# Optimization experiments

Measured on AMD Instinct MI355X. Metric: run time of the kernel, lower is better.

## Reference

```python
import jax, jax.numpy as jnp
import numpy as np

B, S, D = 4, 8192, 1024
H = 16
HD = D // H          # 64
AD = 64              # approx_dim
EPS = 1e-6


def setup_inputs() -> dict:
    key = jax.random.key(0)
    ks = jax.random.split(key, 5)
    x = jax.random.normal(ks[0], (B, S, D), dtype=jnp.float32)
    # qkv_proj: Linear(D, 3*D)
    W_qkv = jax.random.normal(ks[1], (3 * D, D), dtype=jnp.float32) * (1.0 / np.sqrt(D))
    b_qkv = jnp.zeros((3 * D,), dtype=jnp.float32)
    # proj: Linear(HD, AD) with xavier_uniform init, zero bias
    limit = np.sqrt(6.0 / (HD + AD))
    W_p = jax.random.uniform(ks[2], (AD, HD), dtype=jnp.float32, minval=-limit, maxval=limit)
    b_p = jnp.zeros((AD,), dtype=jnp.float32)
    return {"x": x, "W_qkv": W_qkv, "b_qkv": b_qkv, "W_p": W_p, "b_p": b_p}


def reference(x, W_qkv, b_qkv, W_p, b_p):
    # qkv projection and split
    qkv = x @ W_qkv.T + b_qkv                      # [B,S,3D]
    Q, K, V = jnp.split(qkv, 3, axis=-1)
    # [B,S,D] -> [B,H,S,HD]
    def to_heads(t):
        return t.reshape(B, S, H, HD).transpose(0, 2, 1, 3)
    Q, K, V = to_heads(Q), to_heads(K), to_heads(V)
    # shared projection to approx dim, feature map phi(u) = sqrt(1 + u^2)
    pQ = jnp.einsum('bhsd,ad->bhsa', Q, W_p) + b_p
    pK = jnp.einsum('bhsd,ad->bhsa', K, W_p) + b_p
    phi_Q = jnp.sqrt(1.0 + pQ * pQ)                # [B,H,S,AD]
    phi_K = jnp.sqrt(1.0 + pK * pK)
    # linear attention: O(S) chained contractions
    KTV = jnp.einsum('bhsa,bhsv->bhav', phi_K, V)  # [B,H,AD,HD]
    numerator = jnp.einsum('bhsa,bhav->bhsv', phi_Q, KTV)  # [B,H,S,HD]
    k_sum = phi_K.sum(axis=2)                      # [B,H,AD]
    denominator = jnp.einsum('bhsa,bha->bhs', phi_Q, k_sum)  # [B,H,S]
    head_out = numerator / (denominator[..., None] + EPS)
    # [B,H,S,HD] -> [B,S,D]
    return head_out.transpose(0, 2, 1, 3).reshape(B, S, D)
```

## Files before the change

### kernel.cpp

```cpp
#include <hip/hip_runtime.h>
#include <hip/hip_bf16.h>
#include <cstdint>

static constexpr int Bc  = 4;
static constexpr int Sc  = 8192;
static constexpr int Dc  = 1024;
static constexpr int Hc  = 16;
static constexpr int BHc = Bc * Hc;
static constexpr int Mc  = Bc * Sc;
static constexpr int N3c = 3 * Dc;
static constexpr float EPSc = 1e-6f;

using bf16x8 = __attribute__((ext_vector_type(8))) __bf16;
using f32x4  = __attribute__((ext_vector_type(4))) float;

__device__ __forceinline__ ushort f2bf(float f) {
  union { float f; uint32_t u; } v; v.f = f;
  uint32_t u = v.u;
  return (ushort)((u + 0x7fffu + ((u >> 16) & 1u)) >> 16);
}
__device__ __forceinline__ float bf2f(ushort h) {
  union { uint32_t u; float f; } v; v.u = ((uint32_t)h) << 16;
  return v.f;
}

typedef const __attribute__((address_space(1))) unsigned int* gas_u32p;
typedef __attribute__((address_space(3))) unsigned int* las_u32p;
__device__ __forceinline__ void gld_lds16(const void* g, void* l) {
  __builtin_amdgcn_global_load_lds((gas_u32p)g, (las_u32p)l, 16, 0, 0);
}

__global__ __launch_bounds__(256) void prep_k(const float* __restrict__ x,
                                              ushort* __restrict__ xb,
                                              const float* __restrict__ Wq,
                                              const float* __restrict__ Wp,
                                              const float* __restrict__ bq,
                                              const float* __restrict__ bp,
                                              ushort* __restrict__ W3b,
                                              float* __restrict__ bias3) {
  const int t = threadIdx.x;
  if (blockIdx.x < 2048) {
    const int n4 = Mc * Dc / 4;
    for (int i = blockIdx.x * 256 + t; i < n4; i += 2048 * 256) {
      float4 v = reinterpret_cast<const float4*>(x)[i];
      ushort4 o; o.x = f2bf(v.x); o.y = f2bf(v.y); o.z = f2bf(v.z); o.w = f2bf(v.w);
      reinterpret_cast<ushort4*>(xb)[i] = o;
    }
    return;
  }
  const int bx = blockIdx.x - 2048;
  const int p = bx >> 4, h = bx & 15;
  if (p == 2) {
    const int base = 2048 + h * 64;
    for (int li = t; li < 64 * 256; li += 256) {
      int r = li >> 8, c4 = (li & 255) * 4;
      float4 v = *reinterpret_cast<const float4*>(&Wq[(size_t)(base + r) * 1024 + c4]);
      ushort4 o; o.x = f2bf(v.x); o.y = f2bf(v.y); o.z = f2bf(v.z); o.w = f2bf(v.w);
      *reinterpret_cast<ushort4*>(&W3b[(size_t)(base + r) * 1024 + c4]) = o;
    }
    if (t < 64) bias3[base + t] = bq[base + t];
    return;
  }
  __shared__ ushort Ws[64 * 64];
  __shared__ ushort Tq[256 * 64];
  const int rbase = p * 1024 + h * 64;
  for (int li = t; li < 64 * 16; li += 256) {
    int a = li >> 4, h4 = (li & 15) * 4;
    float4 v = *reinterpret_cast<const float4*>(&Wp[a * 64 + h4]);
    ushort4 o; o.x = f2bf(v.x); o.y = f2bf(v.y); o.z = f2bf(v.z); o.w = f2bf(v.w);
    *reinterpret_cast<ushort4*>(&Ws[a * 64 + h4]) = o;
  }
  if (t < 64) {
    float s = bp[t];
    for (int hd = 0; hd < 64; ++hd) s += Wp[t * 64 + hd] * bq[rbase + hd];
    bias3[rbase + t] = s;
  }
  const int w = t >> 6, lane = t & 63, lr = lane & 15, kg = lane >> 4;
  for (int dt = 0; dt < 4; ++dt) {
    __syncthreads();
    for (int li = t; li < 64 * 64; li += 256) {
      int hd = li >> 6, d4 = (li & 63) * 4;
      float4 v = *reinterpret_cast<const float4*>(&Wq[(size_t)(rbase + hd) * 1024 + dt * 256 + d4]);
      Tq[(d4 + 0) * 64 + hd] = f2bf(v.x);
      Tq[(d4 + 1) * 64 + hd] = f2bf(v.y);
      Tq[(d4 + 2) * 64 + hd] = f2bf(v.z);
      Tq[(d4 + 3) * 64 + hd] = f2bf(v.w);
    }
    __syncthreads();
    f32x4 acc[4][4];
#pragma unroll
    for (int i = 0; i < 4; i++)
#pragma unroll
      for (int j = 0; j < 4; j++) acc[i][j] = (f32x4){0.f, 0.f, 0.f, 0.f};
#pragma unroll
    for (int kk = 0; kk < 2; ++kk) {
      bf16x8 af[4], bfr[4];
#pragma unroll
      for (int i = 0; i < 4; i++)
        af[i] = *reinterpret_cast<const bf16x8*>(&Ws[(i * 16 + lr) * 64 + kk * 32 + kg * 8]);
#pragma unroll
      for (int j = 0; j < 4; j++)
        bfr[j] = *reinterpret_cast<const bf16x8*>(&Tq[(w * 64 + j * 16 + lr) * 64 + kk * 32 + kg * 8]);
#pragma unroll
      for (int i = 0; i < 4; i++)
#pragma unroll
        for (int j = 0; j < 4; j++)
          acc[i][j] = __builtin_amdgcn_mfma_f32_16x16x32_bf16(af[i], bfr[j], acc[i][j], 0, 0, 0);
    }
#pragma unroll
    for (int i = 0; i < 4; i++)
#pragma unroll
      for (int j = 0; j < 4; j++)
#pragma unroll
        for (int r = 0; r < 4; r++)
          W3b[(size_t)(rbase + i * 16 + kg * 4 + r) * 1024 + dt * 256 + w * 64 + j * 16 + lr] =
              f2bf(acc[i][j][r]);
  }
}

__global__ __launch_bounds__(512, 2) void gemm_kv_k(const ushort* __restrict__ xb,
                                                    const ushort* __restrict__ W3b,
                                                    const float* __restrict__ bias3,
                                                    ushort* __restrict__ KTb,
                                                    ushort* __restrict__ VTb) {
  __shared__ __align__(16) ushort As[4 * 8192];
  __shared__ __align__(16) ushort Bs[4 * 8192];
  const int t = threadIdx.x, wave = t >> 6, lane = t & 63;
  const int lr = lane & 15, kg = lane >> 4;
  const int wr = wave >> 2, wc = wave & 3;

  const int flat = blockIdx.x;
  const int swz  = (flat & 7) * 128 + (flat >> 3);
  const int n0 = 1024 + (swz % 8) * 256;
  const int m0 = (swz / 8) * 256;

  const int srow = t >> 2;
  const int sg   = (t & 3) ^ ((t >> 3) & 3);
  const int swb  = wave * 512;

  auto STAGE = [&](int tile, int buf) {
    const int kt = tile * 32;
#pragma unroll
    for (int is = 0; is < 2; ++is) {
      gld_lds16(xb  + (size_t)(m0 + is * 128 + srow) * 1024 + kt + sg * 8,
                As + buf * 8192 + is * 4096 + swb);
      gld_lds16(W3b + (size_t)(n0 + is * 128 + srow) * 1024 + kt + sg * 8,
                Bs + buf * 8192 + is * 4096 + swb);
    }
  };

  f32x4 acc[8][4];
#pragma unroll
  for (int f = 0; f < 8; f++)
#pragma unroll
    for (int j = 0; j < 4; j++) acc[f][j] = (f32x4){0.f, 0.f, 0.f, 0.f};

  const int cp = (kg ^ ((lr >> 1) & 3)) * 8;
  const ushort* Ard = As + (wr * 128 + lr) * 32 + cp;
  const ushort* Brd = Bs + (wc * 64 + lr) * 32 + cp;

  auto COMPUTE = [&](int buf) {
    bf16x8 af[8], bfr[4];
    const ushort* Ab = Ard + buf * 8192;
    const ushort* Bb = Brd + buf * 8192;
#pragma unroll
    for (int f = 0; f < 8; f++) af[f] = *reinterpret_cast<const bf16x8*>(Ab + f * 512);
#pragma unroll
    for (int j = 0; j < 4; j++) bfr[j] = *reinterpret_cast<const bf16x8*>(Bb + j * 512);
    __builtin_amdgcn_s_setprio(1);
#pragma unroll
    for (int f = 0; f < 8; f++)
#pragma unroll
      for (int j = 0; j < 4; j++)
        acc[f][j] = __builtin_amdgcn_mfma_f32_16x16x32_bf16(af[f], bfr[j], acc[f][j], 0, 0, 0);
    __builtin_amdgcn_s_setprio(0);
  };

  STAGE(0, 0);
  STAGE(1, 1);
  STAGE(2, 2);
  asm volatile("s_waitcnt vmcnt(8)" ::: "memory");
  __builtin_amdgcn_s_barrier();

#pragma unroll 1
  for (int i = 0; i < 7; ++i) {
    const int tb = i * 4;
#pragma unroll
    for (int j = 0; j < 4; ++j) {
      STAGE(tb + j + 3, (j + 3) & 3);
      COMPUTE(j);
      asm volatile("s_waitcnt vmcnt(8)" ::: "memory");
      __builtin_amdgcn_s_barrier();
    }
  }
  STAGE(31, 3);
  COMPUTE(0);
  asm volatile("s_waitcnt vmcnt(8)" ::: "memory");
  __builtin_amdgcn_s_barrier();
  COMPUTE(1);
  asm volatile("s_waitcnt vmcnt(4)" ::: "memory");
  __builtin_amdgcn_s_barrier();
  COMPUTE(2);
  asm volatile("s_waitcnt vmcnt(0)" ::: "memory");
  __builtin_amdgcn_s_barrier();
  COMPUTE(3);

  const int n0w  = n0 + wc * 64;
  const int part = n0w >> 10;
  const int h    = (n0w & 1023) >> 6;
  const int bq   = m0 >> 13;
  const int s_base = (m0 & 8191) + wr * 128;
  float bias[4];
#pragma unroll
  for (int j = 0; j < 4; j++) bias[j] = bias3[n0w + j * 16 + lr];

  ushort* dst = ((part == 1) ? KTb : VTb) + ((size_t)(bq * Hc + h)) * 64 * Sc;
#pragma unroll
  for (int f = 0; f < 8; f++) {
    const int s = s_base + f * 16 + kg * 4;
#pragma unroll
    for (int j = 0; j < 4; j++) {
      ushort4 o;
      if (part == 1) {
#pragma unroll
        for (int r = 0; r < 4; r++) {
          float p = acc[f][j][r] + bias[j];
          (&o.x)[r] = f2bf(sqrtf(1.f + p * p));
        }
      } else {
#pragma unroll
        for (int r = 0; r < 4; r++) (&o.x)[r] = f2bf(acc[f][j][r] + bias[j]);
      }
      *reinterpret_cast<ushort4*>(&dst[(size_t)(j * 16 + lr) * Sc + s]) = o;
    }
  }
}

__global__ __launch_bounds__(256, 2) void ktv_part_k(const ushort* __restrict__ KT,
                                                     const ushort* __restrict__ VT,
                                                     float* __restrict__ KTVp,
                                                     float* __restrict__ ksump) {
  __shared__ __align__(16) ushort Ks[2 * 8192];
  __shared__ __align__(16) ushort Vs[2 * 8192];
  const int t = threadIdx.x, chunk = blockIdx.x, bh = blockIdx.y;
  const int wave = t >> 6, lane = t & 63, lr = lane & 15, kg = lane >> 4;
  const size_t hb = (size_t)bh * 64 * Sc;
  const int s0 = chunk * 1024;

  f32x4 acc[4];
  f32x4 acc_ks;
#pragma unroll
  for (int j = 0; j < 4; j++) acc[j] = (f32x4){0.f, 0.f, 0.f, 0.f};
  acc_ks = (f32x4){0.f, 0.f, 0.f, 0.f};

  bf16x8 ones;
#pragma unroll
  for (int e = 0; e < 8; e++) ones[e] = (__bf16)1.0f;

  const int srl = t >> 4;
  const int scc = (t & 15) ^ ((t >> 4) & 7);
  const int wb  = (t >> 6) * 512;

  auto STG = [&](int st, int buf) {
    const int sb = s0 + st * 128;
#pragma unroll
    for (int is = 0; is < 4; ++is) {
      const int row = is * 16 + srl;
      gld_lds16(KT + hb + (size_t)row * Sc + sb + scc * 8, Ks + buf * 8192 + is * 2048 + wb);
      gld_lds16(VT + hb + (size_t)row * Sc + sb + scc * 8, Vs + buf * 8192 + is * 2048 + wb);
    }
  };

  auto COMPUTE = [&](int buf) {
    const ushort* Kb = Ks + buf * 8192;
    const ushort* Vb = Vs + buf * 8192;
#pragma unroll
    for (int ks4 = 0; ks4 < 4; ++ks4) {
      const int pos = ((ks4 * 4 + kg) ^ (lr & 7)) * 8;
      bf16x8 af = *reinterpret_cast<const bf16x8*>(Kb + (wave * 16 + lr) * 128 + pos);
      acc_ks = __builtin_amdgcn_mfma_f32_16x16x32_bf16(af, ones, acc_ks, 0, 0, 0);
#pragma unroll
      for (int j = 0; j < 4; ++j) {
        bf16x8 bv = *reinterpret_cast<const bf16x8*>(Vb + (j * 16 + lr) * 128 + pos);
        acc[j] = __builtin_amdgcn_mfma_f32_16x16x32_bf16(af, bv, acc[j], 0, 0, 0);
      }
    }
  };

  STG(0, 0);
  __syncthreads();
#pragma unroll 1
  for (int st = 0; st < 8; ++st) {
    if (st < 7) STG(st + 1, (st + 1) & 1);
    COMPUTE(st & 1);
    __syncthreads();
  }

  float* outp = KTVp + ((size_t)bh * 8 + chunk) * 4096;
#pragma unroll
  for (int j = 0; j < 4; ++j)
#pragma unroll
    for (int r = 0; r < 4; ++r)
      outp[(wave * 16 + kg * 4 + r) * 64 + j * 16 + lr] = acc[j][r];
  if (lr == 0) {
#pragma unroll
    for (int r = 0; r < 4; ++r)
      ksump[((size_t)bh * 8 + chunk) * 64 + wave * 16 + kg * 4 + r] = acc_ks[r];
  }
}

__global__ __launch_bounds__(256) void ktv_red_k(const float* __restrict__ KTVp,
                                                 const float* __restrict__ ksump,
                                                 ushort* __restrict__ KTVTb,
                                                 float* __restrict__ ksum) {
  const int bh = blockIdx.x, t = threadIdx.x;
  for (int li = t; li < 4096; li += 256) {
    const int v = li >> 6, a = li & 63;
    float s = 0.f;
    for (int c = 0; c < 8; c++) s += KTVp[((size_t)bh * 8 + c) * 4096 + a * 64 + v];
    KTVTb[(size_t)bh * 4096 + li] = f2bf(s);
  }
  if (t < 64) {
    float s = 0.f;
    for (int c = 0; c < 8; c++) s += ksump[((size_t)bh * 8 + c) * 64 + t];
    ksum[bh * 64 + t] = s;
  }
}

__global__ __launch_bounds__(512, 2) void gemm_q_k(const ushort* __restrict__ xb,
                                                   const ushort* __restrict__ W3b,
                                                   const float* __restrict__ bias3,
                                                   const ushort* __restrict__ KTVTb,
                                                   const float* __restrict__ ksum,
                                                   float* __restrict__ out) {
  __shared__ __align__(16) ushort As[4 * 8192];
  __shared__ __align__(16) ushort Bs[4 * 8192];
  const int t = threadIdx.x, wave = t >> 6, lane = t & 63;
  const int lr = lane & 15, kg = lane >> 4;
  const int wr = wave >> 2, wc = wave & 3;

  const int flat = blockIdx.x;
  const int swz  = (flat & 7) * 64 + (flat >> 3);
  const int n0 = (swz % 4) * 256;
  const int m0 = (swz / 4) * 256;

  const int srow = t >> 2;
  const int sg   = (t & 3) ^ ((t >> 3) & 3);
  const int swb  = wave * 512;

  auto STAGE = [&](int tile, int buf) {
    const int kt = tile * 32;
#pragma unroll
    for (int is = 0; is < 2; ++is) {
      gld_lds16(xb  + (size_t)(m0 + is * 128 + srow) * 1024 + kt + sg * 8,
                As + buf * 8192 + is * 4096 + swb);
      gld_lds16(W3b + (size_t)(n0 + is * 128 + srow) * 1024 + kt + sg * 8,
                Bs + buf * 8192 + is * 4096 + swb);
    }
  };

  f32x4 acc[8][4];
#pragma unroll
  for (int f = 0; f < 8; f++)
#pragma unroll
    for (int j = 0; j < 4; j++) acc[f][j] = (f32x4){0.f, 0.f, 0.f, 0.f};

  const int cp = (kg ^ ((lr >> 1) & 3)) * 8;
  const ushort* Ard = As + (wr * 128 + lr) * 32 + cp;
  const ushort* Brd = Bs + (wc * 64 + lr) * 32 + cp;

  auto COMPUTE = [&](int buf) {
    bf16x8 af[8], bfr[4];
    const ushort* Ab = Ard + buf * 8192;
    const ushort* Bb = Brd + buf * 8192;
#pragma unroll
    for (int f = 0; f < 8; f++) af[f] = *reinterpret_cast<const bf16x8*>(Ab + f * 512);
#pragma unroll
    for (int j = 0; j < 4; j++) bfr[j] = *reinterpret_cast<const bf16x8*>(Bb + j * 512);
    __builtin_amdgcn_s_setprio(1);
#pragma unroll
    for (int f = 0; f < 8; f++)
#pragma unroll
      for (int j = 0; j < 4; j++)
        acc[f][j] = __builtin_amdgcn_mfma_f32_16x16x32_bf16(af[f], bfr[j], acc[f][j], 0, 0, 0);
    __builtin_amdgcn_s_setprio(0);
  };

  STAGE(0, 0);
  STAGE(1, 1);
  STAGE(2, 2);
  asm volatile("s_waitcnt vmcnt(8)" ::: "memory");
  __builtin_amdgcn_s_barrier();

#pragma unroll 1
  for (int i = 0; i < 7; ++i) {
    const int tb = i * 4;
#pragma unroll
    for (int j = 0; j < 4; ++j) {
      STAGE(tb + j + 3, (j + 3) & 3);
      COMPUTE(j);
      asm volatile("s_waitcnt vmcnt(8)" ::: "memory");
      __builtin_amdgcn_s_barrier();
    }
  }
  STAGE(31, 3);
  COMPUTE(0);
  asm volatile("s_waitcnt vmcnt(8)" ::: "memory");
  __builtin_amdgcn_s_barrier();
  COMPUTE(1);
  asm volatile("s_waitcnt vmcnt(4)" ::: "memory");
  __builtin_amdgcn_s_barrier();
  COMPUTE(2);
  asm volatile("s_waitcnt vmcnt(0)" ::: "memory");
  __builtin_amdgcn_s_barrier();
  COMPUTE(3);

  const int n0w = n0 + wc * 64;
  const int h   = n0w >> 6;
  const int bq  = m0 >> 13;
  const int bh  = bq * Hc + h;
  const int s_base = (m0 & 8191) + wr * 128;
  float bias[4];
#pragma unroll
  for (int j = 0; j < 4; j++) bias[j] = bias3[n0w + j * 16 + lr];

  __syncthreads();
  ushort* ep = (wave < 4) ? (As + wave * 8192) : (Bs + (wave - 4) * 8192);

#pragma unroll
  for (int f = 0; f < 8; f++)
#pragma unroll
    for (int j = 0; j < 4; j++) {
      const int g = j * 2 + (lr >> 3);
      const int cl = lr & 7;
#pragma unroll
      for (int r = 0; r < 4; r++) {
        const int row = f * 16 + kg * 4 + r;
        float p = acc[f][j][r] + bias[j];
        ep[row * 64 + ((g ^ (row & 7)) << 3) + cl] = f2bf(sqrtf(1.f + p * p));
      }
    }

  bf16x8 bfr[4][2];
#pragma unroll
  for (int j = 0; j < 4; j++)
#pragma unroll
    for (int ks = 0; ks < 2; ks++)
      bfr[j][ks] = *reinterpret_cast<const bf16x8*>(
          &KTVTb[(size_t)bh * 4096 + (j * 16 + lr) * 64 + ks * 32 + kg * 8]);
  float ksc[2][8];
#pragma unroll
  for (int ks = 0; ks < 2; ks++) {
    float4 v0 = *reinterpret_cast<const float4*>(&ksum[bh * 64 + ks * 32 + kg * 8]);
    float4 v1 = *reinterpret_cast<const float4*>(&ksum[bh * 64 + ks * 32 + kg * 8 + 4]);
    ksc[ks][0] = v0.x; ksc[ks][1] = v0.y; ksc[ks][2] = v0.z; ksc[ks][3] = v0.w;
    ksc[ks][4] = v1.x; ksc[ks][5] = v1.y; ksc[ks][6] = v1.z; ksc[ks][7] = v1.w;
  }

#pragma unroll 1
  for (int f = 0; f < 8; f++) {
    bf16x8 af[2];
#pragma unroll
    for (int ks = 0; ks < 2; ks++)
      af[ks] = *reinterpret_cast<const bf16x8*>(
          &ep[(f * 16 + lr) * 64 + (((ks * 4 + kg) ^ (lr & 7)) << 3)]);
    float d = 0.f;
#pragma unroll
    for (int ks = 0; ks < 2; ks++)
#pragma unroll
      for (int e = 0; e < 8; e++) d += (float)af[ks][e] * ksc[ks][e];
    d += __shfl_xor(d, 16, 64);
    d += __shfl_xor(d, 32, 64);
    float den[4];
#pragma unroll
    for (int r = 0; r < 4; r++) den[r] = __shfl(d, kg * 4 + r, 64) + EPSc;
    f32x4 nacc[4];
#pragma unroll
    for (int j = 0; j < 4; j++) nacc[j] = (f32x4){0.f, 0.f, 0.f, 0.f};
#pragma unroll
    for (int ks = 0; ks < 2; ks++)
#pragma unroll
      for (int j = 0; j < 4; j++)
        nacc[j] = __builtin_amdgcn_mfma_f32_16x16x32_bf16(af[ks], bfr[j][ks], nacc[j], 0, 0, 0);
#pragma unroll
    for (int j = 0; j < 4; j++)
#pragma unroll
      for (int r = 0; r < 4; r++) {
        const int s = s_base + f * 16 + kg * 4 + r;
        out[((size_t)bq * Sc + s) * 1024 + h * 64 + j * 16 + lr] = nacc[j][r] / den[r];
      }
  }
}

extern "C" void kernel_launch(void* const* d_in, const int* in_sizes, int n_in,
                              void* d_out, int out_size, void* d_ws, size_t ws_size,
                              hipStream_t stream) {
  const float* x     = (const float*)d_in[0];
  const float* W_qkv = (const float*)d_in[1];
  const float* b_qkv = (const float*)d_in[2];
  const float* W_p   = (const float*)d_in[3];
  const float* b_p   = (const float*)d_in[4];
  float* out = (float*)d_out;

  size_t off = 0;
  auto carve = [&](size_t bytes) -> void* {
    void* p = (char*)d_ws + off;
    off += (bytes + 255) & ~(size_t)255;
    return p;
  };
  const size_t headElems = (size_t)BHc * Sc * 64;
  ushort* xb    = (ushort*)carve((size_t)Mc * Dc * 2);
  ushort* KTb   = (ushort*)carve(headElems * 2);
  ushort* VTb   = (ushort*)carve(headElems * 2);
  ushort* W3b   = (ushort*)carve((size_t)N3c * Dc * 2);
  float*  bias3 = (float*)carve((size_t)N3c * 4);
  float*  KTVp  = (float*)carve((size_t)BHc * 8 * 4096 * 4);
  float*  ksmp  = (float*)carve((size_t)BHc * 8 * 64 * 4);
  ushort* KTVTb = (ushort*)carve((size_t)BHc * 4096 * 2);
  float*  ksum  = (float*)carve((size_t)BHc * 64 * 4);
  (void)ws_size; (void)n_in; (void)in_sizes; (void)out_size;

  prep_k<<<2096, 256, 0, stream>>>(x, xb, W_qkv, W_p, b_qkv, b_p, W3b, bias3);
  gemm_kv_k<<<(Mc / 256) * (2048 / 256), 512, 0, stream>>>(xb, W3b, bias3, KTb, VTb);
  ktv_part_k<<<dim3(8, BHc), 256, 0, stream>>>(KTb, VTb, KTVp, ksmp);
  ktv_red_k<<<BHc, 256, 0, stream>>>(KTVp, ksmp, KTVTb, ksum);
  gemm_q_k<<<(Mc / 256) * (1024 / 256), 512, 0, stream>>>(xb, W3b, bias3, KTVTb, ksum, out);
}
```

Measured before the change: 383.8 us.

## Switch GEMM mainloops to double-buffered BK=64 tiles with 8-way swizzle

Both the K/V and Q projection GEMMs now stage 64-wide K tiles into two LDS buffers instead of 32-wide tiles into four. The LDS swizzle changes to an 8-chunk XOR pattern and each compute step issues two MFMA k-substeps per tile. This halves the number of barrier and wait rounds per K loop and gives longer MFMA bursts per barrier. The cost is a shallower prefetch distance (one tile ahead instead of three), which may expose more global load latency.

```diff
diff --git a/kernel.cpp b/kernel.cpp
--- a/kernel.cpp
+++ b/kernel.cpp
@@ -118,13 +118,14 @@
   }
 }
 
+
 __global__ __launch_bounds__(512, 2) void gemm_kv_k(const ushort* __restrict__ xb,
                                                     const ushort* __restrict__ W3b,
                                                     const float* __restrict__ bias3,
                                                     ushort* __restrict__ KTb,
                                                     ushort* __restrict__ VTb) {
-  __shared__ __align__(16) ushort As[4 * 8192];
-  __shared__ __align__(16) ushort Bs[4 * 8192];
+  __shared__ __align__(16) ushort As[2 * 16384];
+  __shared__ __align__(16) ushort Bs[2 * 16384];
   const int t = threadIdx.x, wave = t >> 6, lane = t & 63;
   const int lr = lane & 15, kg = lane >> 4;
   const int wr = wave >> 2, wc = wave & 3;
@@ -134,18 +135,18 @@
   const int n0 = 1024 + (swz % 8) * 256;
   const int m0 = (swz / 8) * 256;
 
-  const int srow = t >> 2;
-  const int sg   = (t & 3) ^ ((t >> 3) & 3);
-  const int swb  = wave * 512;
+  const int srow8 = lane >> 3;
+  const int sg    = (lane & 7) ^ ((lane >> 3) & 7);
 
   auto STAGE = [&](int tile, int buf) {
-    const int kt = tile * 32;
-#pragma unroll
-    for (int is = 0; is < 2; ++is) {
-      gld_lds16(xb  + (size_t)(m0 + is * 128 + srow) * 1024 + kt + sg * 8,
-                As + buf * 8192 + is * 4096 + swb);
-      gld_lds16(W3b + (size_t)(n0 + is * 128 + srow) * 1024 + kt + sg * 8,
-                Bs + buf * 8192 + is * 4096 + swb);
+    const int kt = tile * 64;
+#pragma unroll
+    for (int i = 0; i < 4; ++i) {
+      const int r0 = (wave * 4 + i) * 8;
+      gld_lds16(xb  + (size_t)(m0 + r0 + srow8) * 1024 + kt + sg * 8,
+                As + buf * 16384 + (wave * 4 + i) * 512);
+      gld_lds16(W3b + (size_t)(n0 + r0 + srow8) * 1024 + kt + sg * 8,
+                Bs + buf * 16384 + (wave * 4 + i) * 512);
     }
   };
 
@@ -155,55 +156,54 @@
 #pragma unroll
     for (int j = 0; j < 4; j++) acc[f][j] = (f32x4){0.f, 0.f, 0.f, 0.f};
 
-  const int cp = (kg ^ ((lr >> 1) & 3)) * 8;
-  const ushort* Ard = As + (wr * 128 + lr) * 32 + cp;
-  const ushort* Brd = Bs + (wc * 64 + lr) * 32 + cp;
-
   auto COMPUTE = [&](int buf) {
-    bf16x8 af[8], bfr[4];
-    const ushort* Ab = Ard + buf * 8192;
-    const ushort* Bb = Brd + buf * 8192;
-#pragma unroll
-    for (int f = 0; f < 8; f++) af[f] = *reinterpret_cast<const bf16x8*>(Ab + f * 512);
-#pragma unroll
-    for (int j = 0; j < 4; j++) bfr[j] = *reinterpret_cast<const bf16x8*>(Bb + j * 512);
-    __builtin_amdgcn_s_setprio(1);
-#pragma unroll
-    for (int f = 0; f < 8; f++)
+    const ushort* Ab = As + buf * 16384;
+    const ushort* Bb = Bs + buf * 16384;
+#pragma unroll
+    for (int kk = 0; kk < 2; ++kk) {
+      const int cp = ((kk * 4 + kg) ^ (lr & 7)) * 8;
+      bf16x8 af[8], bfr[4];
+#pragma unroll
+      for (int f = 0; f < 8; f++)
+        af[f] = *reinterpret_cast<const bf16x8*>(Ab + (wr * 128 + f * 16 + lr) * 64 + cp);
 #pragma unroll
       for (int j = 0; j < 4; j++)
-        acc[f][j] = __builtin_amdgcn_mfma_f32_16x16x32_bf16(af[f], bfr[j], acc[f][j], 0, 0, 0);
-    __builtin_amdgcn_s_setprio(0);
+        bfr[j] = *reinterpret_cast<const bf16x8*>(Bb + (wc * 64 + j * 16 + lr) * 64 + cp);
+      __builtin_amdgcn_s_setprio(1);
+#pragma unroll
+      for (int f = 0; f < 8; f++)
+#pragma unroll
+        for (int j = 0; j < 4; j++)
+          acc[f][j] = __builtin_amdgcn_mfma_f32_16x16x32_bf16(af[f], bfr[j], acc[f][j], 0, 0, 0);
+      __builtin_amdgcn_s_setprio(0);
+    }
   };
 
   STAGE(0, 0);
-  STAGE(1, 1);
-  STAGE(2, 2);
+#pragma unroll 1
+  for (int tt = 0; tt < 7; ++tt) {
+    STAGE(tt * 2 + 1, 1);
+    asm volatile("s_waitcnt vmcnt(8)" ::: "memory");
+    __builtin_amdgcn_s_barrier();
+    COMPUTE(0);
+    asm volatile("" ::: "memory");
+    __builtin_amdgcn_s_barrier();
+    STAGE(tt * 2 + 2, 0);
+    asm volatile("s_waitcnt vmcnt(8)" ::: "memory");
+    __builtin_amdgcn_s_barrier();
+    COMPUTE(1);
+    asm volatile("" ::: "memory");
+    __builtin_amdgcn_s_barrier();
+  }
+  STAGE(15, 1);
   asm volatile("s_waitcnt vmcnt(8)" ::: "memory");
   __builtin_amdgcn_s_barrier();
-
-#pragma unroll 1
-  for (int i = 0; i < 7; ++i) {
-    const int tb = i * 4;
-#pragma unroll
-    for (int j = 0; j < 4; ++j) {
-      STAGE(tb + j + 3, (j + 3) & 3);
-      COMPUTE(j);
-      asm volatile("s_waitcnt vmcnt(8)" ::: "memory");
-      __builtin_amdgcn_s_barrier();
-    }
-  }
-  STAGE(31, 3);
   COMPUTE(0);
-  asm volatile("s_waitcnt vmcnt(8)" ::: "memory");
+  asm volatile("" ::: "memory");
+  __builtin_amdgcn_s_barrier();
+  asm volatile("s_waitcnt vmcnt(0)" ::: "memory");
   __builtin_amdgcn_s_barrier();
   COMPUTE(1);
-  asm volatile("s_waitcnt vmcnt(4)" ::: "memory");
-  __builtin_amdgcn_s_barrier();
-  COMPUTE(2);
-  asm volatile("s_waitcnt vmcnt(0)" ::: "memory");
-  __builtin_amdgcn_s_barrier();
-  COMPUTE(3);
 
   const int n0w  = n0 + wc * 64;
   const int part = n0w >> 10;
@@ -333,8 +333,8 @@
                                                    const ushort* __restrict__ KTVTb,
                                                    const float* __restrict__ ksum,
                                                    float* __restrict__ out) {
-  __shared__ __align__(16) ushort As[4 * 8192];
-  __shared__ __align__(16) ushort Bs[4 * 8192];
+  __shared__ __align__(16) ushort As[2 * 16384];
+  __shared__ __align__(16) ushort Bs[2 * 16384];
   const int t = threadIdx.x, wave = t >> 6, lane = t & 63;
   const int lr = lane & 15, kg = lane >> 4;
   const int wr = wave >> 2, wc = wave & 3;
@@ -344,18 +344,18 @@
   const int n0 = (swz % 4) * 256;
   const int m0 = (swz / 4) * 256;
 
-  const int srow = t >> 2;
-  const int sg   = (t & 3) ^ ((t >> 3) & 3);
-  const int swb  = wave * 512;
+  const int srow8 = lane >> 3;
+  const int sg    = (lane & 7) ^ ((lane >> 3) & 7);
 
   auto STAGE = [&](int tile, int buf) {
-    const int kt = tile * 32;
-#pragma unroll
-    for (int is = 0; is < 2; ++is) {
-      gld_lds16(xb  + (size_t)(m0 + is * 128 + srow) * 1024 + kt + sg * 8,
-                As + buf * 8192 + is * 4096 + swb);
-      gld_lds16(W3b + (size_t)(n0 + is * 128 + srow) * 1024 + kt + sg * 8,
-                Bs + buf * 8192 + is * 4096 + swb);
+    const int kt = tile * 64;
+#pragma unroll
+    for (int i = 0; i < 4; ++i) {
+      const int r0 = (wave * 4 + i) * 8;
+      gld_lds16(xb  + (size_t)(m0 + r0 + srow8) * 1024 + kt + sg * 8,
+                As + buf * 16384 + (wave * 4 + i) * 512);
+      gld_lds16(W3b + (size_t)(n0 + r0 + srow8) * 1024 + kt + sg * 8,
+                Bs + buf * 16384 + (wave * 4 + i) * 512);
     }
   };
 
@@ -365,55 +365,54 @@
 #pragma unroll
     for (int j = 0; j < 4; j++) acc[f][j] = (f32x4){0.f, 0.f, 0.f, 0.f};
 
-  const int cp = (kg ^ ((lr >> 1) & 3)) * 8;
-  const ushort* Ard = As + (wr * 128 + lr) * 32 + cp;
-  const ushort* Brd = Bs + (wc * 64 + lr) * 32 + cp;
-
   auto COMPUTE = [&](int buf) {
-    bf16x8 af[8], bfr[4];
-    const ushort* Ab = Ard + buf * 8192;
-    const ushort* Bb = Brd + buf * 8192;
-#pragma unroll
-    for (int f = 0; f < 8; f++) af[f] = *reinterpret_cast<const bf16x8*>(Ab + f * 512);
-#pragma unroll
-    for (int j = 0; j < 4; j++) bfr[j] = *reinterpret_cast<const bf16x8*>(Bb + j * 512);
-    __builtin_amdgcn_s_setprio(1);
-#pragma unroll
-    for (int f = 0; f < 8; f++)
+    const ushort* Ab = As + buf * 16384;
+    const ushort* Bb = Bs + buf * 16384;
+#pragma unroll
+    for (int kk = 0; kk < 2; ++kk) {
+      const int cp = ((kk * 4 + kg) ^ (lr & 7)) * 8;
+      bf16x8 af[8], bfr[4];
+#pragma unroll
+      for (int f = 0; f < 8; f++)
+        af[f] = *reinterpret_cast<const bf16x8*>(Ab + (wr * 128 + f * 16 + lr) * 64 + cp);
 #pragma unroll
       for (int j = 0; j < 4; j++)
-        acc[f][j] = __builtin_amdgcn_mfma_f32_16x16x32_bf16(af[f], bfr[j], acc[f][j], 0, 0, 0);
-    __builtin_amdgcn_s_setprio(0);
+        bfr[j] = *reinterpret_cast<const bf16x8*>(Bb + (wc * 64 + j * 16 + lr) * 64 + cp);
+      __builtin_amdgcn_s_setprio(1);
+#pragma unroll
+      for (int f = 0; f < 8; f++)
+#pragma unroll
+        for (int j = 0; j < 4; j++)
+          acc[f][j] = __builtin_amdgcn_mfma_f32_16x16x32_bf16(af[f], bfr[j], acc[f][j], 0, 0, 0);
+      __builtin_amdgcn_s_setprio(0);
+    }
   };
 
   STAGE(0, 0);
-  STAGE(1, 1);
-  STAGE(2, 2);
+#pragma unroll 1
+  for (int tt = 0; tt < 7; ++tt) {
+    STAGE(tt * 2 + 1, 1);
+    asm volatile("s_waitcnt vmcnt(8)" ::: "memory");
+    __builtin_amdgcn_s_barrier();
+    COMPUTE(0);
+    asm volatile("" ::: "memory");
+    __builtin_amdgcn_s_barrier();
+    STAGE(tt * 2 + 2, 0);
+    asm volatile("s_waitcnt vmcnt(8)" ::: "memory");
+    __builtin_amdgcn_s_barrier();
+    COMPUTE(1);
+    asm volatile("" ::: "memory");
+    __builtin_amdgcn_s_barrier();
+  }
+  STAGE(15, 1);
   asm volatile("s_waitcnt vmcnt(8)" ::: "memory");
   __builtin_amdgcn_s_barrier();
-
-#pragma unroll 1
-  for (int i = 0; i < 7; ++i) {
-    const int tb = i * 4;
-#pragma unroll
-    for (int j = 0; j < 4; ++j) {
-      STAGE(tb + j + 3, (j + 3) & 3);
-      COMPUTE(j);
-      asm volatile("s_waitcnt vmcnt(8)" ::: "memory");
-      __builtin_amdgcn_s_barrier();
-    }
-  }
-  STAGE(31, 3);
   COMPUTE(0);
-  asm volatile("s_waitcnt vmcnt(8)" ::: "memory");
+  asm volatile("" ::: "memory");
+  __builtin_amdgcn_s_barrier();
+  asm volatile("s_waitcnt vmcnt(0)" ::: "memory");
   __builtin_amdgcn_s_barrier();
   COMPUTE(1);
-  asm volatile("s_waitcnt vmcnt(4)" ::: "memory");
-  __builtin_amdgcn_s_barrier();
-  COMPUTE(2);
-  asm volatile("s_waitcnt vmcnt(0)" ::: "memory");
-  __builtin_amdgcn_s_barrier();
-  COMPUTE(3);
 
   const int n0w = n0 + wc * 64;
   const int h   = n0w >> 6;
```

Result: no change. 389.7 us (+1.5%).

## Restructure KV GEMM mainloop into double-buffered 64-wide K tiles with interleaved staging

Applied to the files above, without the earlier changes.

The KV projection GEMM now uses two buffers of 64-wide K tiles, each split into two 32-wide halves, in place of a four-deep ring of 32-wide tiles. Each tile is computed in four quarter steps of 16 MFMAs. Staging loads for the next tile are placed between those steps, separated by compiler-fenced barriers, so LDS reads, global-to-LDS copies and MFMA work interleave more finely. The cost is a shallower prefetch depth and many more barriers per tile, which can leave waves stalled on synchronisation.

```diff
diff --git a/kernel.cpp b/kernel.cpp
--- a/kernel.cpp
+++ b/kernel.cpp
@@ -29,6 +29,8 @@
 __device__ __forceinline__ void gld_lds16(const void* g, void* l) {
   __builtin_amdgcn_global_load_lds((gas_u32p)g, (las_u32p)l, 16, 0, 0);
 }
+
+#define BARF do { asm volatile("" ::: "memory"); __builtin_amdgcn_s_barrier(); asm volatile("" ::: "memory"); } while (0)
 
 __global__ __launch_bounds__(256) void prep_k(const float* __restrict__ x,
                                               ushort* __restrict__ xb,
@@ -138,6 +140,235 @@
   const int sg   = (t & 3) ^ ((t >> 3) & 3);
   const int swb  = wave * 512;
 
+  auto stgA = [&](int tile, int kh) {
+    const int col = tile * 64 + kh * 32 + sg * 8;
+    ushort* dst = As + ((tile & 1) * 2 + kh) * 8192 + swb;
+    gld_lds16(xb + (size_t)(m0 + srow) * 1024 + col, dst);
+    gld_lds16(xb + (size_t)(m0 + 128 + srow) * 1024 + col, dst + 4096);
+  };
+  auto stgB = [&](int tile, int kh) {
+    const int col = tile * 64 + kh * 32 + sg * 8;
+    ushort* dst = Bs + ((tile & 1) * 2 + kh) * 8192 + swb;
+    gld_lds16(W3b + (size_t)(n0 + srow) * 1024 + col, dst);
+    gld_lds16(W3b + (size_t)(n0 + 128 + srow) * 1024 + col, dst + 4096);
+  };
+
+  f32x4 acc[8][4];
+#pragma unroll
+  for (int f = 0; f < 8; f++)
+#pragma unroll
+    for (int j = 0; j < 4; j++) acc[f][j] = (f32x4){0.f, 0.f, 0.f, 0.f};
+
+  const int cp = (kg ^ ((lr >> 1) & 3)) * 8;
+  bf16x8 bfr[4];
+
+  auto readA4 = [&](bf16x8* af, int buf, int fh, int kk) {
+#pragma unroll
+    for (int f = 0; f < 4; f++)
+      af[f] = *reinterpret_cast<const bf16x8*>(
+          As + (buf * 2 + kk) * 8192 + (wr * 128 + fh * 64 + f * 16 + lr) * 32 + cp);
+  };
+  auto readB4 = [&](int buf, int kk) {
+#pragma unroll
+    for (int j = 0; j < 4; j++)
+      bfr[j] = *reinterpret_cast<const bf16x8*>(
+          Bs + (buf * 2 + kk) * 8192 + (wc * 64 + j * 16 + lr) * 32 + cp);
+  };
+  auto mfma16 = [&](const bf16x8* af, int fh) {
+    __builtin_amdgcn_s_setprio(1);
+#pragma unroll
+    for (int f = 0; f < 4; f++)
+#pragma unroll
+      for (int j = 0; j < 4; j++)
+        acc[fh * 4 + f][j] =
+            __builtin_amdgcn_mfma_f32_16x16x32_bf16(af[f], bfr[j], acc[fh * 4 + f][j], 0, 0, 0);
+    __builtin_amdgcn_s_setprio(0);
+  };
+
+  auto TILE = [&](int T, int buf, bool st) {
+    bf16x8 af[4];
+    readB4(buf, 0);
+    readA4(af, buf, 0, 0);
+    if (st) stgA(T + 1, 0);
+    BARF;
+    mfma16(af, 0);
+    BARF;
+    readA4(af, buf, 1, 0);
+    if (st) stgB(T + 1, 0);
+    BARF;
+    mfma16(af, 1);
+    if (st) asm volatile("s_waitcnt vmcnt(4)" ::: "memory");
+    else    asm volatile("s_waitcnt vmcnt(0)" ::: "memory");
+    BARF;
+    readB4(buf, 1);
+    readA4(af, buf, 0, 1);
+    if (st) stgA(T + 1, 1);
+    BARF;
+    mfma16(af, 0);
+    BARF;
+    readA4(af, buf, 1, 1);
+    if (st) stgB(T + 1, 1);
+    BARF;
+    mfma16(af, 1);
+    if (st) asm volatile("s_waitcnt vmcnt(4)" ::: "memory");
+    BARF;
+  };
+
+  stgA(0, 0); stgB(0, 0); stgA(0, 1); stgB(0, 1);
+  asm volatile("s_waitcnt vmcnt(4)" ::: "memory");
+  BARF;
+
+#pragma unroll 1
+  for (int tt = 0; tt < 7; ++tt) {
+    TILE(tt * 2, 0, true);
+    TILE(tt * 2 + 1, 1, true);
+  }
+  TILE(14, 0, true);
+  TILE(15, 1, false);
+
+  const int n0w  = n0 + wc * 64;
+  const int part = n0w >> 10;
+  const int h    = (n0w & 1023) >> 6;
+  const int bq   = m0 >> 13;
+  const int s_base = (m0 & 8191) + wr * 128;
+  float bias[4];
+#pragma unroll
+  for (int j = 0; j < 4; j++) bias[j] = bias3[n0w + j * 16 + lr];
+
+  ushort* dst = ((part == 1) ? KTb : VTb) + ((size_t)(bq * Hc + h)) * 64 * Sc;
+#pragma unroll
+  for (int f = 0; f < 8; f++) {
+    const int s = s_base + f * 16 + kg * 4;
+#pragma unroll
+    for (int j = 0; j < 4; j++) {
+      ushort4 o;
+      if (part == 1) {
+#pragma unroll
+        for (int r = 0; r < 4; r++) {
+          float p = acc[f][j][r] + bias[j];
+          (&o.x)[r] = f2bf(sqrtf(1.f + p * p));
+        }
+      } else {
+#pragma unroll
+        for (int r = 0; r < 4; r++) (&o.x)[r] = f2bf(acc[f][j][r] + bias[j]);
+      }
+      *reinterpret_cast<ushort4*>(&dst[(size_t)(j * 16 + lr) * Sc + s]) = o;
+    }
+  }
+}
+
+__global__ __launch_bounds__(256, 2) void ktv_part_k(const ushort* __restrict__ KT,
+                                                     const ushort* __restrict__ VT,
+                                                     float* __restrict__ KTVp,
+                                                     float* __restrict__ ksump) {
+  __shared__ __align__(16) ushort Ks[2 * 8192];
+  __shared__ __align__(16) ushort Vs[2 * 8192];
+  const int t = threadIdx.x, chunk = blockIdx.x, bh = blockIdx.y;
+  const int wave = t >> 6, lane = t & 63, lr = lane & 15, kg = lane >> 4;
+  const size_t hb = (size_t)bh * 64 * Sc;
+  const int s0 = chunk * 1024;
+
+  f32x4 acc[4];
+  f32x4 acc_ks;
+#pragma unroll
+  for (int j = 0; j < 4; j++) acc[j] = (f32x4){0.f, 0.f, 0.f, 0.f};
+  acc_ks = (f32x4){0.f, 0.f, 0.f, 0.f};
+
+  bf16x8 ones;
+#pragma unroll
+  for (int e = 0; e < 8; e++) ones[e] = (__bf16)1.0f;
+
+  const int srl = t >> 4;
+  const int scc = (t & 15) ^ ((t >> 4) & 7);
+  const int wb  = (t >> 6) * 512;
+
+  auto STG = [&](int st, int buf) {
+    const int sb = s0 + st * 128;
+#pragma unroll
+    for (int is = 0; is < 4; ++is) {
+      const int row = is * 16 + srl;
+      gld_lds16(KT + hb + (size_t)row * Sc + sb + scc * 8, Ks + buf * 8192 + is * 2048 + wb);
+      gld_lds16(VT + hb + (size_t)row * Sc + sb + scc * 8, Vs + buf * 8192 + is * 2048 + wb);
+    }
+  };
+
+  auto COMPUTE = [&](int buf) {
+    const ushort* Kb = Ks + buf * 8192;
+    const ushort* Vb = Vs + buf * 8192;
+#pragma unroll
+    for (int ks4 = 0; ks4 < 4; ++ks4) {
+      const int pos = ((ks4 * 4 + kg) ^ (lr & 7)) * 8;
+      bf16x8 af = *reinterpret_cast<const bf16x8*>(Kb + (wave * 16 + lr) * 128 + pos);
+      acc_ks = __builtin_amdgcn_mfma_f32_16x16x32_bf16(af, ones, acc_ks, 0, 0, 0);
+#pragma unroll
+      for (int j = 0; j < 4; ++j) {
+        bf16x8 bv = *reinterpret_cast<const bf16x8*>(Vb + (j * 16 + lr) * 128 + pos);
+        acc[j] = __builtin_amdgcn_mfma_f32_16x16x32_bf16(af, bv, acc[j], 0, 0, 0);
+      }
+    }
+  };
+
+  STG(0, 0);
+  __syncthreads();
+#pragma unroll 1
+  for (int st = 0; st < 8; ++st) {
+    if (st < 7) STG(st + 1, (st + 1) & 1);
+    COMPUTE(st & 1);
+    __syncthreads();
+  }
+
+  float* outp = KTVp + ((size_t)bh * 8 + chunk) * 4096;
+#pragma unroll
+  for (int j = 0; j < 4; ++j)
+#pragma unroll
+    for (int r = 0; r < 4; ++r)
+      outp[(wave * 16 + kg * 4 + r) * 64 + j * 16 + lr] = acc[j][r];
+  if (lr == 0) {
+#pragma unroll
+    for (int r = 0; r < 4; ++r)
+      ksump[((size_t)bh * 8 + chunk) * 64 + wave * 16 + kg * 4 + r] = acc_ks[r];
+  }
+}
+
+__global__ __launch_bounds__(256) void ktv_red_k(const float* __restrict__ KTVp,
+                                                 const float* __restrict__ ksump,
+                                                 ushort* __restrict__ KTVTb,
+                                                 float* __restrict__ ksum) {
+  const int bh = blockIdx.x, t = threadIdx.x;
+  for (int li = t; li < 4096; li += 256) {
+    const int v = li >> 6, a = li & 63;
+    float s = 0.f;
+    for (int c = 0; c < 8; c++) s += KTVp[((size_t)bh * 8 + c) * 4096 + a * 64 + v];
+    KTVTb[(size_t)bh * 4096 + li] = f2bf(s);
+  }
+  if (t < 64) {
+    float s = 0.f;
+    for (int c = 0; c < 8; c++) s += ksump[((size_t)bh * 8 + c) * 64 + t];
+    ksum[bh * 64 + t] = s;
+  }
+}
+
+__global__ __launch_bounds__(512, 2) void gemm_q_k(const ushort* __restrict__ xb,
+                                                   const ushort* __restrict__ W3b,
+                                                   const float* __restrict__ bias3,
+                                                   const ushort* __restrict__ KTVTb,
+                                                   const float* __restrict__ ksum,
+                                                   float* __restrict__ out) {
+  __shared__ __align__(16) ushort As[4 * 8192];
+  __shared__ __align__(16) ushort Bs[4 * 8192];
+  const int t = threadIdx.x, wave = t >> 6, lane = t & 63;
+  const int lr = lane & 15, kg = lane >> 4;
+  const int wr = wave >> 2, wc = wave & 3;
+
+  const int flat = blockIdx.x;
+  const int swz  = (flat & 7) * 64 + (flat >> 3);
+  const int n0 = (swz % 4) * 256;
+  const int m0 = (swz / 4) * 256;
+
+  const int srow = t >> 2;
+  const int sg   = (t & 3) ^ ((t >> 3) & 3);
+  const int swb  = wave * 512;
+
   auto STAGE = [&](int tile, int buf) {
     const int kt = tile * 32;
 #pragma unroll
@@ -205,216 +436,6 @@
   __builtin_amdgcn_s_barrier();
   COMPUTE(3);
 
-  const int n0w  = n0 + wc * 64;
-  const int part = n0w >> 10;
-  const int h    = (n0w & 1023) >> 6;
-  const int bq   = m0 >> 13;
-  const int s_base = (m0 & 8191) + wr * 128;
-  float bias[4];
-#pragma unroll
-  for (int j = 0; j < 4; j++) bias[j] = bias3[n0w + j * 16 + lr];
-
-  ushort* dst = ((part == 1) ? KTb : VTb) + ((size_t)(bq * Hc + h)) * 64 * Sc;
-#pragma unroll
-  for (int f = 0; f < 8; f++) {
-    const int s = s_base + f * 16 + kg * 4;
-#pragma unroll
-    for (int j = 0; j < 4; j++) {
-      ushort4 o;
-      if (part == 1) {
-#pragma unroll
-        for (int r = 0; r < 4; r++) {
-          float p = acc[f][j][r] + bias[j];
-          (&o.x)[r] = f2bf(sqrtf(1.f + p * p));
-        }
-      } else {
-#pragma unroll
-        for (int r = 0; r < 4; r++) (&o.x)[r] = f2bf(acc[f][j][r] + bias[j]);
-      }
-      *reinterpret_cast<ushort4*>(&dst[(size_t)(j * 16 + lr) * Sc + s]) = o;
-    }
-  }
-}
-
-__global__ __launch_bounds__(256, 2) void ktv_part_k(const ushort* __restrict__ KT,
-                                                     const ushort* __restrict__ VT,
-                                                     float* __restrict__ KTVp,
-                                                     float* __restrict__ ksump) {
-  __shared__ __align__(16) ushort Ks[2 * 8192];
-  __shared__ __align__(16) ushort Vs[2 * 8192];
-  const int t = threadIdx.x, chunk = blockIdx.x, bh = blockIdx.y;
-  const int wave = t >> 6, lane = t & 63, lr = lane & 15, kg = lane >> 4;
-  const size_t hb = (size_t)bh * 64 * Sc;
-  const int s0 = chunk * 1024;
-
-  f32x4 acc[4];
-  f32x4 acc_ks;
-#pragma unroll
-  for (int j = 0; j < 4; j++) acc[j] = (f32x4){0.f, 0.f, 0.f, 0.f};
-  acc_ks = (f32x4){0.f, 0.f, 0.f, 0.f};
-
-  bf16x8 ones;
-#pragma unroll
-  for (int e = 0; e < 8; e++) ones[e] = (__bf16)1.0f;
-
-  const int srl = t >> 4;
-  const int scc = (t & 15) ^ ((t >> 4) & 7);
-  const int wb  = (t >> 6) * 512;
-
-  auto STG = [&](int st, int buf) {
-    const int sb = s0 + st * 128;
-#pragma unroll
-    for (int is = 0; is < 4; ++is) {
-      const int row = is * 16 + srl;
-      gld_lds16(KT + hb + (size_t)row * Sc + sb + scc * 8, Ks + buf * 8192 + is * 2048 + wb);
-      gld_lds16(VT + hb + (size_t)row * Sc + sb + scc * 8, Vs + buf * 8192 + is * 2048 + wb);
-    }
-  };
-
-  auto COMPUTE = [&](int buf) {
-    const ushort* Kb = Ks + buf * 8192;
-    const ushort* Vb = Vs + buf * 8192;
-#pragma unroll
-    for (int ks4 = 0; ks4 < 4; ++ks4) {
-      const int pos = ((ks4 * 4 + kg) ^ (lr & 7)) * 8;
-      bf16x8 af = *reinterpret_cast<const bf16x8*>(Kb + (wave * 16 + lr) * 128 + pos);
-      acc_ks = __builtin_amdgcn_mfma_f32_16x16x32_bf16(af, ones, acc_ks, 0, 0, 0);
-#pragma unroll
-      for (int j = 0; j < 4; ++j) {
-        bf16x8 bv = *reinterpret_cast<const bf16x8*>(Vb + (j * 16 + lr) * 128 + pos);
-        acc[j] = __builtin_amdgcn_mfma_f32_16x16x32_bf16(af, bv, acc[j], 0, 0, 0);
-      }
-    }
-  };
-
-  STG(0, 0);
-  __syncthreads();
-#pragma unroll 1
-  for (int st = 0; st < 8; ++st) {
-    if (st < 7) STG(st + 1, (st + 1) & 1);
-    COMPUTE(st & 1);
-    __syncthreads();
-  }
-
-  float* outp = KTVp + ((size_t)bh * 8 + chunk) * 4096;
-#pragma unroll
-  for (int j = 0; j < 4; ++j)
-#pragma unroll
-    for (int r = 0; r < 4; ++r)
-      outp[(wave * 16 + kg * 4 + r) * 64 + j * 16 + lr] = acc[j][r];
-  if (lr == 0) {
-#pragma unroll
-    for (int r = 0; r < 4; ++r)
-      ksump[((size_t)bh * 8 + chunk) * 64 + wave * 16 + kg * 4 + r] = acc_ks[r];
-  }
-}
-
-__global__ __launch_bounds__(256) void ktv_red_k(const float* __restrict__ KTVp,
-                                                 const float* __restrict__ ksump,
-                                                 ushort* __restrict__ KTVTb,
-                                                 float* __restrict__ ksum) {
-  const int bh = blockIdx.x, t = threadIdx.x;
-  for (int li = t; li < 4096; li += 256) {
-    const int v = li >> 6, a = li & 63;
-    float s = 0.f;
-    for (int c = 0; c < 8; c++) s += KTVp[((size_t)bh * 8 + c) * 4096 + a * 64 + v];
-    KTVTb[(size_t)bh * 4096 + li] = f2bf(s);
-  }
-  if (t < 64) {
-    float s = 0.f;
-    for (int c = 0; c < 8; c++) s += ksump[((size_t)bh * 8 + c) * 64 + t];
-    ksum[bh * 64 + t] = s;
-  }
-}
-
-__global__ __launch_bounds__(512, 2) void gemm_q_k(const ushort* __restrict__ xb,
-                                                   const ushort* __restrict__ W3b,
-                                                   const float* __restrict__ bias3,
-                                                   const ushort* __restrict__ KTVTb,
-                                                   const float* __restrict__ ksum,
-                                                   float* __restrict__ out) {
-  __shared__ __align__(16) ushort As[4 * 8192];
-  __shared__ __align__(16) ushort Bs[4 * 8192];
-  const int t = threadIdx.x, wave = t >> 6, lane = t & 63;
-  const int lr = lane & 15, kg = lane >> 4;
-  const int wr = wave >> 2, wc = wave & 3;
-
-  const int flat = blockIdx.x;
-  const int swz  = (flat & 7) * 64 + (flat >> 3);
-  const int n0 = (swz % 4) * 256;
-  const int m0 = (swz / 4) * 256;
-
-  const int srow = t >> 2;
-  const int sg   = (t & 3) ^ ((t >> 3) & 3);
-  const int swb  = wave * 512;
-
-  auto STAGE = [&](int tile, int buf) {
-    const int kt = tile * 32;
-#pragma unroll
-    for (int is = 0; is < 2; ++is) {
-      gld_lds16(xb  + (size_t)(m0 + is * 128 + srow) * 1024 + kt + sg * 8,
-                As + buf * 8192 + is * 4096 + swb);
-      gld_lds16(W3b + (size_t)(n0 + is * 128 + srow) * 1024 + kt + sg * 8,
-                Bs + buf * 8192 + is * 4096 + swb);
-    }
-  };
-
-  f32x4 acc[8][4];
-#pragma unroll
-  for (int f = 0; f < 8; f++)
-#pragma unroll
-    for (int j = 0; j < 4; j++) acc[f][j] = (f32x4){0.f, 0.f, 0.f, 0.f};
-
-  const int cp = (kg ^ ((lr >> 1) & 3)) * 8;
-  const ushort* Ard = As + (wr * 128 + lr) * 32 + cp;
-  const ushort* Brd = Bs + (wc * 64 + lr) * 32 + cp;
-
-  auto COMPUTE = [&](int buf) {
-    bf16x8 af[8], bfr[4];
-    const ushort* Ab = Ard + buf * 8192;
-    const ushort* Bb = Brd + buf * 8192;
-#pragma unroll
-    for (int f = 0; f < 8; f++) af[f] = *reinterpret_cast<const bf16x8*>(Ab + f * 512);
-#pragma unroll
-    for (int j = 0; j < 4; j++) bfr[j] = *reinterpret_cast<const bf16x8*>(Bb + j * 512);
-    __builtin_amdgcn_s_setprio(1);
-#pragma unroll
-    for (int f = 0; f < 8; f++)
-#pragma unroll
-      for (int j = 0; j < 4; j++)
-        acc[f][j] = __builtin_amdgcn_mfma_f32_16x16x32_bf16(af[f], bfr[j], acc[f][j], 0, 0, 0);
-    __builtin_amdgcn_s_setprio(0);
-  };
-
-  STAGE(0, 0);
-  STAGE(1, 1);
-  STAGE(2, 2);
-  asm volatile("s_waitcnt vmcnt(8)" ::: "memory");
-  __builtin_amdgcn_s_barrier();
-
-#pragma unroll 1
-  for (int i = 0; i < 7; ++i) {
-    const int tb = i * 4;
-#pragma unroll
-    for (int j = 0; j < 4; ++j) {
-      STAGE(tb + j + 3, (j + 3) & 3);
-      COMPUTE(j);
-      asm volatile("s_waitcnt vmcnt(8)" ::: "memory");
-      __builtin_amdgcn_s_barrier();
-    }
-  }
-  STAGE(31, 3);
-  COMPUTE(0);
-  asm volatile("s_waitcnt vmcnt(8)" ::: "memory");
-  __builtin_amdgcn_s_barrier();
-  COMPUTE(1);
-  asm volatile("s_waitcnt vmcnt(4)" ::: "memory");
-  __builtin_amdgcn_s_barrier();
-  COMPUTE(2);
-  asm volatile("s_waitcnt vmcnt(0)" ::: "memory");
-  __builtin_amdgcn_s_barrier();
-  COMPUTE(3);
-
   const int n0w = n0 + wc * 64;
   const int h   = n0w >> 6;
   const int bq  = m0 >> 13;
```

Result: no change. 385.2 us (+0.4%).
